# Kernel optimization log

Hardware: AMD Instinct MI355X
Metric: run time of the kernel (lower is better)

Reference implementation:

```python
import jax, jax.numpy as jnp
import numpy as np

NUM_HEADS = 12


def setup_inputs() -> dict:
    key = jax.random.key(0)
    ks = jax.random.split(key, 5)
    B, N, C = 64, 388, 768  # N = 8*8*2 + 16*16 + 4
    return {
        "x": jax.random.normal(ks[0], (B, N, C), dtype=jnp.float32),
        "qkv_w": jax.random.normal(ks[1], (3 * C, C), dtype=jnp.float32) * 0.02,
        "qkv_b": jax.random.normal(ks[2], (3 * C,), dtype=jnp.float32) * 0.02,
        "proj_w": jax.random.normal(ks[3], (C, C), dtype=jnp.float32) * 0.02,
        "proj_b": jax.random.normal(ks[4], (C,), dtype=jnp.float32) * 0.02,
        "t_h": 8, "t_w": 8, "s_h": 16, "s_w": 16,
    }


def reference(x, qkv_w, qkv_b, proj_w, proj_b, t_h, t_w, s_h, s_w):
    B, N, C = x.shape
    H = NUM_HEADS
    D = C // H
    scale = D ** -0.5
    L_t = t_h * t_w * 2          # template (x2) tokens
    L_s = s_h * s_w + 4          # search tokens + 4 extra

    qkv = x @ qkv_w.T + qkv_b                       # [B,N,3C]
    qkv = qkv.reshape(B, N, 3, H, D).transpose(2, 0, 3, 1, 4)  # [3,B,H,N,D]
    q, k, v = qkv[0], qkv[1], qkv[2]                # each [B,H,N,D]

    q_mt, q_s = q[:, :, :L_t], q[:, :, L_t:]
    k_mt = k[:, :, :L_t]
    v_mt = v[:, :, :L_t]

    # template self-attention (template queries attend only to template keys)
    attn_mt = jax.nn.softmax(jnp.einsum("bhqd,bhkd->bhqk", q_mt, k_mt) * scale, axis=-1)
    x_mt = jnp.einsum("bhqk,bhkd->bhqd", attn_mt, v_mt)  # [B,H,L_t,D]
    x_mt = x_mt.transpose(0, 2, 1, 3).reshape(B, L_t, C)

    # search queries attend to ALL keys
    attn_s = jax.nn.softmax(jnp.einsum("bhqd,bhkd->bhqk", q_s, k) * scale, axis=-1)
    x_s = jnp.einsum("bhqk,bhkd->bhqd", attn_s, v)  # [B,H,L_s,D]
    x_s = x_s.transpose(0, 2, 1, 3).reshape(B, L_s, C)

    out = jnp.concatenate([x_mt, x_s], axis=1)      # [B,N,C]
    out = out @ proj_w.T + proj_b
    return out
```

## Files before the change

### kernel.cpp

```cpp
#include <hip/hip_runtime.h>
#include <cstdint>
#include <cstddef>
#include <cmath>

typedef __attribute__((ext_vector_type(4))) float f32x4;
typedef __attribute__((ext_vector_type(8))) short bf16x8;

typedef const __attribute__((address_space(1))) void* gas_ptr;
typedef __attribute__((address_space(3))) void* las_ptr;

static __device__ __forceinline__ short f2bf(float f) {
    __bf16 h = (__bf16)f;
    return __builtin_bit_cast(short, h);
}

constexpr int MP = 25088;

__global__ void cvt_f32_bf16(const float* __restrict__ src, short* __restrict__ dst, int n4) {
    int i = blockIdx.x * blockDim.x + threadIdx.x;
    const int stride = gridDim.x * blockDim.x;
    for (; i < n4; i += stride) {
        const float4 v = reinterpret_cast<const float4*>(src)[i];
        short4 o;
        o.x = f2bf(v.x); o.y = f2bf(v.y); o.z = f2bf(v.z); o.w = f2bf(v.w);
        reinterpret_cast<short4*>(dst)[i] = o;
    }
}

__global__ void cvt_x_pad(const float* __restrict__ src, short* __restrict__ dst) {
    constexpr int N4 = MP * 768 / 4;
    int i = blockIdx.x * blockDim.x + threadIdx.x;
    const int stride = gridDim.x * blockDim.x;
    for (; i < N4; i += stride) {
        const int flat = i * 4;
        const int mp  = flat / 768;
        const int col = flat - mp * 768;
        const int b   = mp / 392;
        const int nn  = mp - b * 392;
        short4 o;
        if (nn < 388) {
            const float4 v = *reinterpret_cast<const float4*>(
                src + ((size_t)(b * 388 + nn) * 768 + col));
            o.x = f2bf(v.x); o.y = f2bf(v.y); o.z = f2bf(v.z); o.w = f2bf(v.w);
        } else {
            o.x = 0; o.y = 0; o.z = 0; o.w = 0;
        }
        reinterpret_cast<short4*>(dst)[i] = o;
    }
}

template<int MODE>
__global__ __launch_bounds__(256) void gemm_bt(
    const short* __restrict__ A, const short* __restrict__ Bw,
    const float* __restrict__ bias,
    short* __restrict__ qk, short* __restrict__ vT,
    float* __restrict__ fo, int NB)
{
    constexpr int K = 768;
    constexpr int KT = 12;
    __shared__ __align__(16) short ldsraw[2 * 128 * 64 * 2];
    short* ldsA = ldsraw;
    short* ldsB = ldsraw + 2 * 128 * 64;

    const int tid  = threadIdx.x;
    const int lane = tid & 63;
    const int wid  = tid >> 6;
    const int lrow = lane & 15;
    const int lgrp = lane >> 4;
    const int wr   = wid >> 1;
    const int wc   = wid & 1;

    const int nwg = gridDim.x;
    const int q8  = nwg >> 3, r8 = nwg & 7;
    const int xcd = blockIdx.x & 7, bidx = blockIdx.x >> 3;
    const int wgid = (xcd < r8 ? xcd * (q8 + 1) : r8 * (q8 + 1) + (xcd - r8) * q8) + bidx;

    int m0, n0;
    if constexpr (MODE == 0) {
        constexpr int G = 14, SG = G * 18;
        const int mg = wgid / SG;
        const int r  = wgid - mg * SG;
        const int n  = r / G;
        const int mi = r - n * G;
        m0 = (mg * G + mi) * 128;
        n0 = n * 128;
    } else {
        m0 = (wgid / NB) * 128;
        n0 = (wgid % NB) * 128;
    }

    f32x4 acc[4][4];
    #pragma unroll
    for (int i = 0; i < 4; ++i)
        #pragma unroll
        for (int j = 0; j < 4; ++j)
            acc[i][j] = f32x4{0.f, 0.f, 0.f, 0.f};

    auto stage = [&](int kt, int buf) {
        #pragma unroll
        for (int it = 0; it < 4; ++it) {
            const int c   = it * 256 + wid * 64 + lane;
            const int row = c >> 3;
            const int scb = ((c & 7) * 16) ^ ((row & 7) << 4);
            const short* ga = A  + (size_t)(m0 + row) * K + kt * 64 + (scb >> 1);
            const short* gb = Bw + (size_t)(n0 + row) * K + kt * 64 + (scb >> 1);
            __builtin_amdgcn_global_load_lds((gas_ptr)ga, (las_ptr)((char*)(ldsA + buf * 128 * 64) + c * 16), 16, 0, 0);
            __builtin_amdgcn_global_load_lds((gas_ptr)gb, (las_ptr)((char*)(ldsB + buf * 128 * 64) + c * 16), 16, 0, 0);
        }
    };

    stage(0, 0);

    for (int kt = 0; kt < KT; ++kt) {
        const int cur = kt & 1;
        if (kt + 1 < KT) {
            stage(kt + 1, cur ^ 1);
            asm volatile("s_waitcnt vmcnt(8)" ::: "memory");
        } else {
            asm volatile("s_waitcnt vmcnt(0)" ::: "memory");
        }
        __builtin_amdgcn_s_barrier();
        __builtin_amdgcn_sched_barrier(0);

        #pragma unroll
        for (int ks = 0; ks < 2; ++ks) {
            bf16x8 af[4], bfv[4];
            #pragma unroll
            for (int i = 0; i < 4; ++i) {
                const int r   = wr * 64 + i * 16 + lrow;
                const int byt = r * 128 + ((ks * 64 + lgrp * 16) ^ ((r & 7) << 4));
                af[i] = *reinterpret_cast<const bf16x8*>((const char*)(ldsA + cur * 128 * 64) + byt);
            }
            #pragma unroll
            for (int j = 0; j < 4; ++j) {
                const int r   = wc * 64 + j * 16 + lrow;
                const int byt = r * 128 + ((ks * 64 + lgrp * 16) ^ ((r & 7) << 4));
                bfv[j] = *reinterpret_cast<const bf16x8*>((const char*)(ldsB + cur * 128 * 64) + byt);
            }
            #pragma unroll
            for (int i = 0; i < 4; ++i)
                #pragma unroll
                for (int j = 0; j < 4; ++j)
                    acc[i][j] = __builtin_amdgcn_mfma_f32_16x16x32_bf16(af[i], bfv[j], acc[i][j], 0, 0, 0);
        }

        __builtin_amdgcn_sched_barrier(0);
        __builtin_amdgcn_s_barrier();
    }

    const int mb = m0 + wr * 64;
    const int nb = n0 + wc * 64;
    if constexpr (MODE == 0) {
        if (n0 < 1536) {
            #pragma unroll
            for (int j = 0; j < 4; ++j) {
                const int c  = nb + j * 16 + lrow;
                const float sc = (c < 768) ? 0.18033688011116f : 1.0f;
                const float bv = bias[c];
                #pragma unroll
                for (int i = 0; i < 4; ++i) {
                    #pragma unroll
                    for (int r = 0; r < 4; ++r) {
                        const int m = mb + i * 16 + lgrp * 4 + r;
                        qk[(size_t)m * 1536 + c] = f2bf((acc[i][j][r] + bv) * sc);
                    }
                }
            }
        } else {
            const int h = (nb - 1536) >> 6;
            short* lw = ldsraw + wid * (64 * 80);
            #pragma unroll
            for (int j = 0; j < 4; ++j) {
                const int dloc = j * 16 + lrow;
                const float bv = bias[nb + j * 16 + lrow];
                #pragma unroll
                for (int i = 0; i < 4; ++i)
                    #pragma unroll
                    for (int r = 0; r < 4; ++r)
                        lw[dloc * 80 + i * 16 + lgrp * 4 + r] = f2bf(acc[i][j][r] + bv);
            }
            asm volatile("s_waitcnt lgkmcnt(0)" ::: "memory");
            __builtin_amdgcn_sched_barrier(0);
            #pragma unroll
            for (int w = 0; w < 8; ++w) {
                const int d    = w * 8 + (lane >> 3);
                const int nloc = (lane & 7) * 8;
                const bf16x8 val = *reinterpret_cast<const bf16x8*>(lw + d * 80 + nloc);
                const int mchunk = mb + nloc;
                const int b  = mchunk / 392;
                const int nn = mchunk - b * 392;
                short* dst = vT + ((size_t)(b * 12 + h) * 64 + d) * 392 + nn;
                *reinterpret_cast<bf16x8*>(dst) = val;
            }
        }
    } else {
        #pragma unroll
        for (int i = 0; i < 4; ++i) {
            #pragma unroll
            for (int r = 0; r < 4; ++r) {
                const int m = mb + i * 16 + lgrp * 4 + r;
                #pragma unroll
                for (int j = 0; j < 4; ++j) {
                    const int c = nb + j * 16 + lrow;
                    fo[(size_t)m * 768 + c] = acc[i][j][r] + bias[c];
                }
            }
        }
    }
}

constexpr int PSTRB = 256;

template<int NT, bool VLDS>
static __device__ __forceinline__ void attn_chunk_lds(
    int kbeg, int k_len,
    const short* __restrict__ klds, const short* __restrict__ vlds,
    const short* __restrict__ vglob,
    const bf16x8 (&qf)[2], char* __restrict__ my,
    int lrow, int lgrp,
    float (&rs)[4], f32x4 (&oacc)[4])
{
    f32x4 sacc[NT];
    #pragma unroll
    for (int t = 0; t < NT; ++t) sacc[t] = f32x4{0.f, 0.f, 0.f, 0.f};

    #pragma unroll
    for (int t = 0; t < NT; ++t) {
        const int kl   = t * 16 + lrow;
        const int byt0 = kl * 128 + ((lgrp * 16) ^ ((kl & 7) << 4));
        const int byt1 = kl * 128 + ((64 + lgrp * 16) ^ ((kl & 7) << 4));
        const bf16x8 k0 = *reinterpret_cast<const bf16x8*>((const char*)klds + byt0);
        const bf16x8 k1 = *reinterpret_cast<const bf16x8*>((const char*)klds + byt1);
        sacc[t] = __builtin_amdgcn_mfma_f32_16x16x32_bf16(qf[0], k0, sacc[t], 0, 0, 0);
        sacc[t] = __builtin_amdgcn_mfma_f32_16x16x32_bf16(qf[1], k1, sacc[t], 0, 0, 0);
    }
    #pragma unroll
    for (int t = 0; t < NT; ++t) {
        const bool bad = (kbeg + t * 16 + lrow >= k_len);
        #pragma unroll
        for (int r = 0; r < 4; ++r) {
            const float p = bad ? 0.f : exp2f(sacc[t][r]);
            rs[r] += p;
            const int row = lgrp * 4 + r;
            const int byt = row * PSTRB + ((t * 32 + lrow * 2) ^ ((row & 7) << 4));
            *reinterpret_cast<short*>(my + byt) = f2bf(p);
        }
    }

    #pragma unroll
    for (int ks = 0; ks < NT / 2; ++ks) {
        const bf16x8 pf = *reinterpret_cast<const bf16x8*>(
            my + lrow * PSTRB + ((ks * 64 + lgrp * 16) ^ ((lrow & 7) << 4)));
        #pragma unroll
        for (int dt = 0; dt < 4; ++dt) {
            const int d = dt * 16 + lrow;
            const bf16x8 vf = VLDS
                ? *reinterpret_cast<const bf16x8*>((const char*)vlds + d * 256 + ((ks * 64 + lgrp * 16) ^ ((d & 7) << 4)))
                : *reinterpret_cast<const bf16x8*>(vglob + (size_t)d * 392 + ks * 32 + lgrp * 8);
            oacc[dt] = __builtin_amdgcn_mfma_f32_16x16x32_bf16(pf, vf, oacc[dt], 0, 0, 0);
        }
    }
}

__global__ __launch_bounds__(256, 2) void attn_flash(
    const short* __restrict__ qkb, const short* __restrict__ vT,
    short* __restrict__ ao)
{
    __shared__ __align__(16) short klds[2][128 * 64];
    __shared__ __align__(16) short vlds[2][64 * 128];
    __shared__ __align__(16) char  plds[4][16 * PSTRB];

    const int tid  = threadIdx.x;
    const int lane = tid & 63;
    const int wid  = tid >> 6;
    const int lrow = lane & 15;
    const int lgrp = lane >> 4;

    const int blk = blockIdx.x;
    const int xcd = blk & 7;
    const int i7  = blk >> 3;
    const int bh  = xcd * 96 + i7 / 7;
    const int bx  = i7 % 7;

    int q_start, qend, k_len, nfull;
    bool tail;
    if (bx < 2) { q_start = bx * 64;             qend = 128; k_len = 128; nfull = 1; tail = false; }
    else        { q_start = 128 + (bx - 2) * 64; qend = 388; k_len = 388; nfull = 3; tail = true;  }

    const int q0 = q_start + wid * 16;

    const int b = bh / 12, h = bh - b * 12;
    const short* qbase = qkb + (size_t)b * 392 * 1536 + h * 64;
    const short* kbase = qbase + 768;
    const short* vbase = vT + (size_t)bh * 64 * 392;

    int qrow = q0 + lrow; if (qrow >= qend) qrow = qend - 1;
    bf16x8 qf[2];
    #pragma unroll
    for (int ks = 0; ks < 2; ++ks)
        qf[ks] = *reinterpret_cast<const bf16x8*>(qbase + (size_t)qrow * 1536 + ks * 32 + lgrp * 8);

    float rs[4] = {0.f, 0.f, 0.f, 0.f};
    f32x4 oacc[4];
    #pragma unroll
    for (int dt = 0; dt < 4; ++dt) oacc[dt] = f32x4{0.f, 0.f, 0.f, 0.f};

    char* my = &plds[wid][0];

    auto stage_full = [&](int ch, int buf) {
        const int kbeg = ch * 128;
        #pragma unroll
        for (int it = 0; it < 4; ++it) {
            const int c = it * 256 + tid;
            const int krow = c >> 3;
            const int kscb = ((c & 7) * 16) ^ ((krow & 7) << 4);
            const short* gk = kbase + (size_t)(kbeg + krow) * 1536 + (kscb >> 1);
            __builtin_amdgcn_global_load_lds((gas_ptr)gk, (las_ptr)((char*)&klds[buf][0] + c * 16), 16, 0, 0);
            const int vrow = c >> 4;
            const int vscb = ((c & 15) * 16) ^ ((vrow & 7) << 4);
            const short* gv = vbase + (size_t)vrow * 392 + kbeg + (vscb >> 1);
            __builtin_amdgcn_global_load_lds((gas_ptr)gv, (las_ptr)((char*)&vlds[buf][0] + c * 16), 16, 0, 0);
        }
    };

    stage_full(0, 0);

    for (int ch = 0; ch < nfull; ++ch) {
        const int cur = ch & 1;
        if (ch + 1 < nfull) {
            stage_full(ch + 1, cur ^ 1);
            asm volatile("s_waitcnt vmcnt(8)" ::: "memory");
        } else {
            asm volatile("s_waitcnt vmcnt(0)" ::: "memory");
        }
        __builtin_amdgcn_s_barrier();
        __builtin_amdgcn_sched_barrier(0);

        attn_chunk_lds<8, true>(ch * 128, k_len, &klds[cur][0], &vlds[cur][0],
                                nullptr, qf, my, lrow, lgrp, rs, oacc);

        __builtin_amdgcn_sched_barrier(0);
        __builtin_amdgcn_s_barrier();
    }

    if (tail) {
        {
            const int c = tid;
            const int krow = c >> 3;
            const int kscb = ((c & 7) * 16) ^ ((krow & 7) << 4);
            int g = 384 + krow; if (g > 391) g = 391;
            const short* gk = kbase + (size_t)g * 1536 + (kscb >> 1);
            __builtin_amdgcn_global_load_lds((gas_ptr)gk, (las_ptr)((char*)&klds[0][0] + c * 16), 16, 0, 0);
        }
        asm volatile("s_waitcnt vmcnt(0)" ::: "memory");
        __builtin_amdgcn_s_barrier();
        __builtin_amdgcn_sched_barrier(0);

        attn_chunk_lds<2, false>(384, k_len, &klds[0][0], nullptr, vbase + 384,
                                 qf, my, lrow, lgrp, rs, oacc);
    }

    #pragma unroll
    for (int msk = 1; msk < 16; msk <<= 1)
        #pragma unroll
        for (int r = 0; r < 4; ++r) rs[r] += __shfl_xor(rs[r], msk, 64);

    float inv[4];
    #pragma unroll
    for (int r = 0; r < 4; ++r) inv[r] = 1.0f / rs[r];
    #pragma unroll
    for (int r = 0; r < 4; ++r) {
        const int qn = q0 + lgrp * 4 + r;
        if (qn < qend) {
            #pragma unroll
            for (int dt = 0; dt < 4; ++dt)
                ao[((size_t)b * 388 + qn) * 768 + h * 64 + dt * 16 + lrow] =
                    f2bf(oacc[dt][r] * inv[r]);
        }
    }
}

extern "C" void kernel_launch(void* const* d_in, const int* in_sizes, int n_in,
                              void* d_out, int out_size, void* d_ws, size_t ws_size,
                              hipStream_t stream) {
    (void)in_sizes; (void)n_in; (void)out_size; (void)ws_size;
    const float* x      = (const float*)d_in[0];
    const float* qkv_w  = (const float*)d_in[1];
    const float* qkv_b  = (const float*)d_in[2];
    const float* proj_w = (const float*)d_in[3];
    const float* proj_b = (const float*)d_in[4];
    float* out = (float*)d_out;

    char* ws = (char*)d_ws;
    short* xb   = (short*)(ws);
    short* attn = (short*)(ws);
    short* qkb  = (short*)(ws + 38535168);
    short* vTb  = (short*)(ws + 115605504);
    short* qwb  = (short*)(ws + 154140672);
    short* pwb  = (short*)(ws + 157679616);

    cvt_x_pad  <<<2048, 256, 0, stream>>>(x, xb);
    cvt_f32_bf16<<<512,  256, 0, stream>>>(qkv_w,  qwb, 2304 * 768 / 4);
    cvt_f32_bf16<<<256,  256, 0, stream>>>(proj_w, pwb, 768 * 768 / 4);

    gemm_bt<0><<<dim3(196 * 18), 256, 0, stream>>>(xb, qwb, qkv_b, qkb, vTb, nullptr, 18);

    attn_flash<<<dim3(5376), 256, 0, stream>>>(qkb, vTb, attn);

    gemm_bt<1><<<dim3(194 * 6), 256, 0, stream>>>(attn, pwb, proj_b, nullptr, nullptr, out, 6);
}
```

Before: 241.0 us.

## Shrink attention KV chunks to 64 keys and raise occupancy to four blocks

Each attention chunk now covers 64 keys instead of 128, so the double-buffered K/V/P shared-memory footprint shrinks. Launch bounds rise from 2 to 4 blocks per CU to hide latency. The separate tail path, which read V straight from global memory, is dropped; the last partial chunk goes through the same LDS pipeline with clamped K rows and key masking. The cost is more barriers and chunk iterations per block. The last chunk's V loads also run past the 392-wide row, relying on masked probabilities being zero.

```diff
diff --git a/kernel.cpp b/kernel.cpp
--- a/kernel.cpp
+++ b/kernel.cpp
@@ -209,23 +209,21 @@
     }
 }
 
-constexpr int PSTRB = 256;
-
-template<int NT, bool VLDS>
-static __device__ __forceinline__ void attn_chunk_lds(
+constexpr int PSTRB = 128;
+
+static __device__ __forceinline__ void attn_chunk64(
     int kbeg, int k_len,
     const short* __restrict__ klds, const short* __restrict__ vlds,
-    const short* __restrict__ vglob,
     const bf16x8 (&qf)[2], char* __restrict__ my,
     int lrow, int lgrp,
     float (&rs)[4], f32x4 (&oacc)[4])
 {
-    f32x4 sacc[NT];
-    #pragma unroll
-    for (int t = 0; t < NT; ++t) sacc[t] = f32x4{0.f, 0.f, 0.f, 0.f};
-
-    #pragma unroll
-    for (int t = 0; t < NT; ++t) {
+    f32x4 sacc[4];
+    #pragma unroll
+    for (int t = 0; t < 4; ++t) sacc[t] = f32x4{0.f, 0.f, 0.f, 0.f};
+
+    #pragma unroll
+    for (int t = 0; t < 4; ++t) {
         const int kl   = t * 16 + lrow;
         const int byt0 = kl * 128 + ((lgrp * 16) ^ ((kl & 7) << 4));
         const int byt1 = kl * 128 + ((64 + lgrp * 16) ^ ((kl & 7) << 4));
@@ -235,7 +233,7 @@
         sacc[t] = __builtin_amdgcn_mfma_f32_16x16x32_bf16(qf[1], k1, sacc[t], 0, 0, 0);
     }
     #pragma unroll
-    for (int t = 0; t < NT; ++t) {
+    for (int t = 0; t < 4; ++t) {
         const bool bad = (kbeg + t * 16 + lrow >= k_len);
         #pragma unroll
         for (int r = 0; r < 4; ++r) {
@@ -248,26 +246,25 @@
     }
 
     #pragma unroll
-    for (int ks = 0; ks < NT / 2; ++ks) {
+    for (int ks = 0; ks < 2; ++ks) {
         const bf16x8 pf = *reinterpret_cast<const bf16x8*>(
             my + lrow * PSTRB + ((ks * 64 + lgrp * 16) ^ ((lrow & 7) << 4)));
         #pragma unroll
         for (int dt = 0; dt < 4; ++dt) {
             const int d = dt * 16 + lrow;
-            const bf16x8 vf = VLDS
-                ? *reinterpret_cast<const bf16x8*>((const char*)vlds + d * 256 + ((ks * 64 + lgrp * 16) ^ ((d & 7) << 4)))
-                : *reinterpret_cast<const bf16x8*>(vglob + (size_t)d * 392 + ks * 32 + lgrp * 8);
+            const bf16x8 vf = *reinterpret_cast<const bf16x8*>(
+                (const char*)vlds + d * 128 + ((ks * 64 + lgrp * 16) ^ ((d & 7) << 4)));
             oacc[dt] = __builtin_amdgcn_mfma_f32_16x16x32_bf16(pf, vf, oacc[dt], 0, 0, 0);
         }
     }
 }
 
-__global__ __launch_bounds__(256, 2) void attn_flash(
+__global__ __launch_bounds__(256, 4) void attn_flash(
     const short* __restrict__ qkb, const short* __restrict__ vT,
     short* __restrict__ ao)
 {
-    __shared__ __align__(16) short klds[2][128 * 64];
-    __shared__ __align__(16) short vlds[2][64 * 128];
+    __shared__ __align__(16) short klds[2][64 * 64];
+    __shared__ __align__(16) short vlds[2][64 * 64];
     __shared__ __align__(16) char  plds[4][16 * PSTRB];
 
     const int tid  = threadIdx.x;
@@ -282,10 +279,9 @@
     const int bh  = xcd * 96 + i7 / 7;
     const int bx  = i7 % 7;
 
-    int q_start, qend, k_len, nfull;
-    bool tail;
-    if (bx < 2) { q_start = bx * 64;             qend = 128; k_len = 128; nfull = 1; tail = false; }
-    else        { q_start = 128 + (bx - 2) * 64; qend = 388; k_len = 388; nfull = 3; tail = true;  }
+    int q_start, qend, k_len, nch;
+    if (bx < 2) { q_start = bx * 64;             qend = 128; k_len = 128; nch = 2; }
+    else        { q_start = 128 + (bx - 2) * 64; qend = 388; k_len = 388; nch = 7; }
 
     const int q0 = q_start + wid * 16;
 
@@ -307,57 +303,45 @@
 
     char* my = &plds[wid][0];
 
-    auto stage_full = [&](int ch, int buf) {
-        const int kbeg = ch * 128;
-        #pragma unroll
-        for (int it = 0; it < 4; ++it) {
+    auto stage64 = [&](int ch, int buf) {
+        const int kbeg = ch * 64;
+        #pragma unroll
+        for (int it = 0; it < 2; ++it) {
             const int c = it * 256 + tid;
             const int krow = c >> 3;
-            const int kscb = ((c & 7) * 16) ^ ((krow & 7) << 4);
-            const short* gk = kbase + (size_t)(kbeg + krow) * 1536 + (kscb >> 1);
+            const int scb = ((c & 7) * 16) ^ ((krow & 7) << 4);
+            int g = kbeg + krow; if (g > 391) g = 391;
+            const short* gk = kbase + (size_t)g * 1536 + (scb >> 1);
             __builtin_amdgcn_global_load_lds((gas_ptr)gk, (las_ptr)((char*)&klds[buf][0] + c * 16), 16, 0, 0);
-            const int vrow = c >> 4;
-            const int vscb = ((c & 15) * 16) ^ ((vrow & 7) << 4);
-            const short* gv = vbase + (size_t)vrow * 392 + kbeg + (vscb >> 1);
+        }
+        #pragma unroll
+        for (int it = 0; it < 2; ++it) {
+            const int c = it * 256 + tid;
+            const int vrow = c >> 3;
+            const int scb = ((c & 7) * 16) ^ ((vrow & 7) << 4);
+            const short* gv = vbase + (size_t)vrow * 392 + kbeg + (scb >> 1);
             __builtin_amdgcn_global_load_lds((gas_ptr)gv, (las_ptr)((char*)&vlds[buf][0] + c * 16), 16, 0, 0);
         }
     };
 
-    stage_full(0, 0);
-
-    for (int ch = 0; ch < nfull; ++ch) {
+    stage64(0, 0);
+
+    for (int ch = 0; ch < nch; ++ch) {
         const int cur = ch & 1;
-        if (ch + 1 < nfull) {
-            stage_full(ch + 1, cur ^ 1);
-            asm volatile("s_waitcnt vmcnt(8)" ::: "memory");
+        if (ch + 1 < nch) {
+            stage64(ch + 1, cur ^ 1);
+            asm volatile("s_waitcnt vmcnt(4)" ::: "memory");
         } else {
             asm volatile("s_waitcnt vmcnt(0)" ::: "memory");
         }
         __builtin_amdgcn_s_barrier();
         __builtin_amdgcn_sched_barrier(0);
 
-        attn_chunk_lds<8, true>(ch * 128, k_len, &klds[cur][0], &vlds[cur][0],
-                                nullptr, qf, my, lrow, lgrp, rs, oacc);
+        attn_chunk64(ch * 64, k_len, &klds[cur][0], &vlds[cur][0],
+                     qf, my, lrow, lgrp, rs, oacc);
 
         __builtin_amdgcn_sched_barrier(0);
         __builtin_amdgcn_s_barrier();
-    }
-
-    if (tail) {
-        {
-            const int c = tid;
-            const int krow = c >> 3;
-            const int kscb = ((c & 7) * 16) ^ ((krow & 7) << 4);
-            int g = 384 + krow; if (g > 391) g = 391;
-            const short* gk = kbase + (size_t)g * 1536 + (kscb >> 1);
-            __builtin_amdgcn_global_load_lds((gas_ptr)gk, (las_ptr)((char*)&klds[0][0] + c * 16), 16, 0, 0);
-        }
-        asm volatile("s_waitcnt vmcnt(0)" ::: "memory");
-        __builtin_amdgcn_s_barrier();
-        __builtin_amdgcn_sched_barrier(0);
-
-        attn_chunk_lds<2, false>(384, k_len, &klds[0][0], nullptr, vbase + 384,
-                                 qf, my, lrow, lgrp, rs, oacc);
     }
 
     #pragma unroll
```

After: 230.0 us. 4.5% less time.
